# Performance work log

Measured on AMD Instinct MI355X. Metric: run time of the kernel, lower is better.

## Reference

```python
import jax, jax.numpy as jnp
import numpy as np

N_CLUSTERS = 512
TEMPERATURE = 0.1


def setup_inputs() -> dict:
    key = jax.random.key(0)
    k1, k2 = jax.random.split(key)
    x = jax.random.normal(k1, (32, 1024, 256), dtype=jnp.float32)
    centroids = jax.random.normal(k2, (N_CLUSTERS, 256), dtype=jnp.float32)
    return {"x": x, "centroids": centroids}


def reference(x, centroids):
    # Flatten non-cluster axes into a sample axis: [N, D]
    B, S, D = x.shape
    xf = x.reshape(-1, D)  # [N, D]
    x_sq = jnp.sum(xf * xf, axis=-1, keepdims=True)           # [N, 1]
    c_sq = jnp.sum(centroids * centroids, axis=-1)             # [K]
    cross = jnp.einsum('nd,kd->nk', xf, centroids)             # [N, K]
    dists = x_sq - 2.0 * cross + c_sq[None, :]                 # [N, K]
    # Temperature-scaled soft assignments
    assignments = jax.nn.softmax(-dists / TEMPERATURE, axis=-1)  # [N, K]
    # Restore leading (non-feature) dims, append cluster axis
    return assignments.reshape(B, S, N_CLUSTERS)
```

## Files before the change

kernel.cpp:

```cpp
#include <hip/hip_runtime.h>

#define NROWS 32768
#define KC 512
#define DDIM 256
#define BM 128
#define BK 32
#define KCH (DDIM / BK)

typedef __attribute__((ext_vector_type(8))) short bf16x8;
typedef __attribute__((ext_vector_type(4))) float f32x4;

union U8 { unsigned short u[8]; bf16x8 v; };

__device__ __forceinline__ unsigned short f2bf(float f) {
    union { float f; unsigned int u; } a; a.f = f;
    unsigned int r = a.u + 0x7fffu + ((a.u >> 16) & 1u);
    return (unsigned short)(r >> 16);
}
__device__ __forceinline__ float bf2f(unsigned short h) {
    union { unsigned int u; float f; } a; a.u = ((unsigned int)h) << 16;
    return a.f;
}

__global__ __launch_bounds__(64) void prep_c(const float* __restrict__ c,
                                             unsigned short* __restrict__ bhi,
                                             unsigned short* __restrict__ blo,
                                             float* __restrict__ csq10) {
    const int n = blockIdx.x, lane = threadIdx.x;
    const int d0 = lane * 4;
    float4 v = ((const float4*)(c + (size_t)n * DDIM))[lane];
    float vv[4] = {v.x, v.y, v.z, v.w};
    unsigned short hh[4], ll[4];
    float ssq = 0.f;
    #pragma unroll
    for (int i = 0; i < 4; ++i) {
        ssq += vv[i] * vv[i];
        hh[i] = f2bf(vv[i]);
        ll[i] = f2bf(vv[i] - bf2f(hh[i]));
    }
    #pragma unroll
    for (int off = 32; off; off >>= 1) ssq += __shfl_xor(ssq, off);
    if (lane == 0) csq10[n] = 10.f * ssq;
    const int ks = d0 >> 5;
    const int q  = (d0 >> 3) & 3;
    const int t  = n >> 4, cc = n & 15;
    const size_t dst = ((size_t)(ks * 32 + t) * 64 + (q * 16 + cc)) * 8 + (d0 & 7);
    *(ushort4*)(bhi + dst) = make_ushort4(hh[0], hh[1], hh[2], hh[3]);
    *(ushort4*)(blo + dst) = make_ushort4(ll[0], ll[1], ll[2], ll[3]);
}

__global__ __launch_bounds__(512, 2) void kmeans_mfma(
    const float* __restrict__ x, const unsigned short* __restrict__ bhi,
    const unsigned short* __restrict__ blo, const float* __restrict__ csq10,
    float* __restrict__ out) {
    __shared__ __align__(16) float lbuf[32 * 516];
    __shared__ float red[2][2][BM];

    const int tid  = threadIdx.x;
    const int w    = tid >> 6, lane = tid & 63;
    const int wm   = w >> 1, wn = w & 1;
    const int cc   = lane & 15, q = lane >> 4;
    const int row0 = blockIdx.x * BM;

    f32x4 acc[2][16];
    #pragma unroll
    for (int mt = 0; mt < 2; ++mt)
        #pragma unroll
        for (int t = 0; t < 16; ++t) acc[mt][t] = (f32x4){0.f, 0.f, 0.f, 0.f};

    const float* xA0 = x + (size_t)(row0 + wm * 32 + cc) * DDIM + q * 8;
    const float* xA1 = xA0 + (size_t)16 * DDIM;

    float4 c00 = *(const float4*)xA0;
    float4 c01 = *(const float4*)(xA0 + 4);
    float4 c10 = *(const float4*)xA1;
    float4 c11 = *(const float4*)(xA1 + 4);

    for (int ks = 0; ks < KCH; ++ks) {
        float4 n00, n01, n10, n11;
        if (ks < KCH - 1) {
            const int kn = (ks + 1) * BK;
            n00 = *(const float4*)(xA0 + kn);
            n01 = *(const float4*)(xA0 + kn + 4);
            n10 = *(const float4*)(xA1 + kn);
            n11 = *(const float4*)(xA1 + kn + 4);
        }
        bf16x8 ah[2], al[2];
        {
            float v0[8] = {c00.x, c00.y, c00.z, c00.w, c01.x, c01.y, c01.z, c01.w};
            float v1[8] = {c10.x, c10.y, c10.z, c10.w, c11.x, c11.y, c11.z, c11.w};
            U8 H0, L0, H1, L1;
            #pragma unroll
            for (int e = 0; e < 8; ++e) {
                H0.u[e] = f2bf(v0[e]); L0.u[e] = f2bf(v0[e] - bf2f(H0.u[e]));
                H1.u[e] = f2bf(v1[e]); L1.u[e] = f2bf(v1[e] - bf2f(H1.u[e]));
            }
            ah[0] = H0.v; al[0] = L0.v; ah[1] = H1.v; al[1] = L1.v;
        }
        const unsigned short* bhp = bhi + ((size_t)(ks * 32 + wn * 16) << 9) + lane * 8;
        const unsigned short* blp = blo + ((size_t)(ks * 32 + wn * 16) << 9) + lane * 8;
        bf16x8 pb[2][2][2];
        pb[0][0][0] = *(const bf16x8*)(bhp);
        pb[0][0][1] = *(const bf16x8*)(blp);
        pb[0][1][0] = *(const bf16x8*)(bhp + 512);
        pb[0][1][1] = *(const bf16x8*)(blp + 512);
        #pragma unroll
        for (int tg = 0; tg < 8; ++tg) {
            const int par = tg & 1, nxt = par ^ 1;
            if (tg < 7) {
                pb[nxt][0][0] = *(const bf16x8*)(bhp + (2 * tg + 2) * 512);
                pb[nxt][0][1] = *(const bf16x8*)(blp + (2 * tg + 2) * 512);
                pb[nxt][1][0] = *(const bf16x8*)(bhp + (2 * tg + 3) * 512);
                pb[nxt][1][1] = *(const bf16x8*)(blp + (2 * tg + 3) * 512);
            }
            #pragma unroll
            for (int tt = 0; tt < 2; ++tt) {
                const int t = 2 * tg + tt;
                bf16x8 bh = pb[par][tt][0];
                bf16x8 bl = pb[par][tt][1];
                acc[0][t] = __builtin_amdgcn_mfma_f32_16x16x32_bf16(ah[0], bh, acc[0][t], 0, 0, 0);
                acc[1][t] = __builtin_amdgcn_mfma_f32_16x16x32_bf16(ah[1], bh, acc[1][t], 0, 0, 0);
                acc[0][t] = __builtin_amdgcn_mfma_f32_16x16x32_bf16(ah[0], bl, acc[0][t], 0, 0, 0);
                acc[1][t] = __builtin_amdgcn_mfma_f32_16x16x32_bf16(ah[1], bl, acc[1][t], 0, 0, 0);
                acc[0][t] = __builtin_amdgcn_mfma_f32_16x16x32_bf16(al[0], bh, acc[0][t], 0, 0, 0);
                acc[1][t] = __builtin_amdgcn_mfma_f32_16x16x32_bf16(al[1], bh, acc[1][t], 0, 0, 0);
            }
        }
        c00 = n00; c01 = n01; c10 = n10; c11 = n11;
    }

    float csqv[16];
    #pragma unroll
    for (int t = 0; t < 16; ++t) csqv[t] = csq10[wn * 256 + t * 16 + cc];
    const int rb = wm * 32 + q * 4;
    float M[2][4], I[2][4];
    #pragma unroll
    for (int mt = 0; mt < 2; ++mt)
        #pragma unroll
        for (int g = 0; g < 4; ++g) {
            float pm = -1e30f;
            #pragma unroll
            for (int t = 0; t < 16; ++t) pm = fmaxf(pm, 20.f * acc[mt][t][g] - csqv[t]);
            #pragma unroll
            for (int off = 1; off < 16; off <<= 1) pm = fmaxf(pm, __shfl_xor(pm, off));
            if (cc == 0) red[0][wn][rb + mt * 16 + g] = pm;
            M[mt][g] = pm;
        }
    __syncthreads();
    #pragma unroll
    for (int mt = 0; mt < 2; ++mt)
        #pragma unroll
        for (int g = 0; g < 4; ++g) {
            M[mt][g] = fmaxf(M[mt][g], red[0][1 - wn][rb + mt * 16 + g]);
            float ps = 0.f;
            #pragma unroll
            for (int t = 0; t < 16; ++t) ps += __expf(20.f * acc[mt][t][g] - csqv[t] - M[mt][g]);
            #pragma unroll
            for (int off = 1; off < 16; off <<= 1) ps += __shfl_xor(ps, off);
            if (cc == 0) red[1][wn][rb + mt * 16 + g] = ps;
        }
    __syncthreads();
    #pragma unroll
    for (int mt = 0; mt < 2; ++mt)
        #pragma unroll
        for (int g = 0; g < 4; ++g)
            I[mt][g] = 1.f / (red[1][0][rb + mt * 16 + g] + red[1][1][rb + mt * 16 + g]);

    #pragma unroll
    for (int p = 0; p < 4; ++p) {
        if (wm == p) {
            #pragma unroll
            for (int mt = 0; mt < 2; ++mt)
                #pragma unroll
                for (int g = 0; g < 4; ++g) {
                    const int   lr = mt * 16 + q * 4 + g;
                    const float mg = M[mt][g], ig = I[mt][g];
                    #pragma unroll
                    for (int t = 0; t < 16; ++t)
                        lbuf[lr * 516 + wn * 256 + t * 16 + cc] =
                            __expf(20.f * acc[mt][t][g] - csqv[t] - mg) * ig;
                }
        }
        __syncthreads();
        #pragma unroll
        for (int j = 0; j < 8; ++j) {
            const int f    = j * 512 + tid;
            const int lrow = f >> 7;
            const int c4   = f & 127;
            float4    v    = *(const float4*)&lbuf[lrow * 516 + c4 * 4];
            *(float4*)(out + (size_t)(row0 + p * 32 + lrow) * KC + c4 * 4) = v;
        }
        __syncthreads();
    }
}

extern "C" void kernel_launch(void* const* d_in, const int* in_sizes, int n_in,
                              void* d_out, int out_size, void* d_ws, size_t ws_size,
                              hipStream_t stream) {
    const float* x   = (const float*)d_in[0];
    const float* c   = (const float*)d_in[1];
    float*       out = (float*)d_out;

    unsigned short* bhi   = (unsigned short*)d_ws;
    unsigned short* blo   = bhi + (size_t)KCH * KC * BK;
    float*          csq10 = (float*)(blo + (size_t)KCH * KC * BK);

    prep_c<<<KC, 64, 0, stream>>>(c, bhi, blo, csq10);
    kmeans_mfma<<<NROWS / BM, 512, 0, stream>>>(x, bhi, blo, csq10, out);
}
```

Measured before the change: 123.3 us.

## Shrink row tile to 32 with four column-split waves and cross-ks B prefetch

The row block drops from 128 to 32 rows per workgroup, and the workgroup goes from 512 to 256 threads. Each of the four waves now covers 128 centroid columns instead of 256, so 1024 blocks are launched instead of 256, the LDS staging buffer shrinks, and accumulator registers fall by half. The B-fragment double buffer is carried across ks iterations so the next chunk's loads overlap the current MFMAs, and the MFMA issue order is regrouped by precision pass. In exchange, each block reloads the full centroid operand from L2 for only 32 rows, which raises global read traffic, and the softmax reductions now span four waves.

```diff
diff --git a/kernel.cpp b/kernel.cpp
--- a/kernel.cpp
+++ b/kernel.cpp
@@ -3,7 +3,7 @@
 #define NROWS 32768
 #define KC 512
 #define DDIM 256
-#define BM 128
+#define BM 32
 #define BK 32
 #define KCH (DDIM / BK)
 
@@ -49,28 +49,34 @@
     *(ushort4*)(blo + dst) = make_ushort4(ll[0], ll[1], ll[2], ll[3]);
 }
 
-__global__ __launch_bounds__(512, 2) void kmeans_mfma(
+__global__ __launch_bounds__(256, 3) void kmeans_mfma(
     const float* __restrict__ x, const unsigned short* __restrict__ bhi,
     const unsigned short* __restrict__ blo, const float* __restrict__ csq10,
     float* __restrict__ out) {
-    __shared__ __align__(16) float lbuf[32 * 516];
-    __shared__ float red[2][2][BM];
+    __shared__ __align__(16) float lbuf[16 * 516];
+    __shared__ float red[2][4][BM];
 
     const int tid  = threadIdx.x;
-    const int w    = tid >> 6, lane = tid & 63;
-    const int wm   = w >> 1, wn = w & 1;
+    const int wn   = tid >> 6, lane = tid & 63;
     const int cc   = lane & 15, q = lane >> 4;
     const int row0 = blockIdx.x * BM;
 
-    f32x4 acc[2][16];
-    #pragma unroll
-    for (int mt = 0; mt < 2; ++mt)
-        #pragma unroll
-        for (int t = 0; t < 16; ++t) acc[mt][t] = (f32x4){0.f, 0.f, 0.f, 0.f};
-
-    const float* xA0 = x + (size_t)(row0 + wm * 32 + cc) * DDIM + q * 8;
+    f32x4 acc[2][8];
+    #pragma unroll
+    for (int mt = 0; mt < 2; ++mt)
+        #pragma unroll
+        for (int t = 0; t < 8; ++t) acc[mt][t] = (f32x4){0.f, 0.f, 0.f, 0.f};
+
+    const float* xA0 = x + (size_t)(row0 + cc) * DDIM + q * 8;
     const float* xA1 = xA0 + (size_t)16 * DDIM;
 
+    const unsigned short* bhp = bhi + ((size_t)(wn * 8) << 9) + lane * 8;
+    const unsigned short* blp = blo + ((size_t)(wn * 8) << 9) + lane * 8;
+    bf16x8 pb[2][2][2];
+    pb[0][0][0] = *(const bf16x8*)(bhp);
+    pb[0][0][1] = *(const bf16x8*)(blp);
+    pb[0][1][0] = *(const bf16x8*)(bhp + 512);
+    pb[0][1][1] = *(const bf16x8*)(blp + 512);
     float4 c00 = *(const float4*)xA0;
     float4 c01 = *(const float4*)(xA0 + 4);
     float4 c10 = *(const float4*)xA1;
@@ -97,42 +103,41 @@
             }
             ah[0] = H0.v; al[0] = L0.v; ah[1] = H1.v; al[1] = L1.v;
         }
-        const unsigned short* bhp = bhi + ((size_t)(ks * 32 + wn * 16) << 9) + lane * 8;
-        const unsigned short* blp = blo + ((size_t)(ks * 32 + wn * 16) << 9) + lane * 8;
-        bf16x8 pb[2][2][2];
-        pb[0][0][0] = *(const bf16x8*)(bhp);
-        pb[0][0][1] = *(const bf16x8*)(blp);
-        pb[0][1][0] = *(const bf16x8*)(bhp + 512);
-        pb[0][1][1] = *(const bf16x8*)(blp + 512);
-        #pragma unroll
-        for (int tg = 0; tg < 8; ++tg) {
+        #pragma unroll
+        for (int tg = 0; tg < 4; ++tg) {
             const int par = tg & 1, nxt = par ^ 1;
-            if (tg < 7) {
+            if (tg < 3) {
                 pb[nxt][0][0] = *(const bf16x8*)(bhp + (2 * tg + 2) * 512);
                 pb[nxt][0][1] = *(const bf16x8*)(blp + (2 * tg + 2) * 512);
                 pb[nxt][1][0] = *(const bf16x8*)(bhp + (2 * tg + 3) * 512);
                 pb[nxt][1][1] = *(const bf16x8*)(blp + (2 * tg + 3) * 512);
+            } else if (ks < KCH - 1) {
+                pb[nxt][0][0] = *(const bf16x8*)(bhp + 32 * 512);
+                pb[nxt][0][1] = *(const bf16x8*)(blp + 32 * 512);
+                pb[nxt][1][0] = *(const bf16x8*)(bhp + 33 * 512);
+                pb[nxt][1][1] = *(const bf16x8*)(blp + 33 * 512);
             }
             #pragma unroll
-            for (int tt = 0; tt < 2; ++tt) {
-                const int t = 2 * tg + tt;
-                bf16x8 bh = pb[par][tt][0];
-                bf16x8 bl = pb[par][tt][1];
-                acc[0][t] = __builtin_amdgcn_mfma_f32_16x16x32_bf16(ah[0], bh, acc[0][t], 0, 0, 0);
-                acc[1][t] = __builtin_amdgcn_mfma_f32_16x16x32_bf16(ah[1], bh, acc[1][t], 0, 0, 0);
-                acc[0][t] = __builtin_amdgcn_mfma_f32_16x16x32_bf16(ah[0], bl, acc[0][t], 0, 0, 0);
-                acc[1][t] = __builtin_amdgcn_mfma_f32_16x16x32_bf16(ah[1], bl, acc[1][t], 0, 0, 0);
-                acc[0][t] = __builtin_amdgcn_mfma_f32_16x16x32_bf16(al[0], bh, acc[0][t], 0, 0, 0);
-                acc[1][t] = __builtin_amdgcn_mfma_f32_16x16x32_bf16(al[1], bh, acc[1][t], 0, 0, 0);
-            }
-        }
+            for (int p = 0; p < 3; ++p)
+                #pragma unroll
+                for (int tt = 0; tt < 2; ++tt) {
+                    const int t = 2 * tg + tt;
+                    const bf16x8 a0 = (p == 2) ? al[0] : ah[0];
+                    const bf16x8 a1 = (p == 2) ? al[1] : ah[1];
+                    const bf16x8 b  = (p == 1) ? pb[par][tt][1] : pb[par][tt][0];
+                    acc[0][t] = __builtin_amdgcn_mfma_f32_16x16x32_bf16(a0, b, acc[0][t], 0, 0, 0);
+                    acc[1][t] = __builtin_amdgcn_mfma_f32_16x16x32_bf16(a1, b, acc[1][t], 0, 0, 0);
+                }
+        }
+        bhp += 32 * 512;
+        blp += 32 * 512;
         c00 = n00; c01 = n01; c10 = n10; c11 = n11;
     }
 
-    float csqv[16];
-    #pragma unroll
-    for (int t = 0; t < 16; ++t) csqv[t] = csq10[wn * 256 + t * 16 + cc];
-    const int rb = wm * 32 + q * 4;
+    float csqv[8];
+    #pragma unroll
+    for (int t = 0; t < 8; ++t) csqv[t] = csq10[wn * 128 + t * 16 + cc];
+    const int rb = q * 4;
     float M[2][4], I[2][4];
     #pragma unroll
     for (int mt = 0; mt < 2; ++mt)
@@ -140,55 +145,57 @@
         for (int g = 0; g < 4; ++g) {
             float pm = -1e30f;
             #pragma unroll
-            for (int t = 0; t < 16; ++t) pm = fmaxf(pm, 20.f * acc[mt][t][g] - csqv[t]);
+            for (int t = 0; t < 8; ++t) pm = fmaxf(pm, 20.f * acc[mt][t][g] - csqv[t]);
             #pragma unroll
             for (int off = 1; off < 16; off <<= 1) pm = fmaxf(pm, __shfl_xor(pm, off));
             if (cc == 0) red[0][wn][rb + mt * 16 + g] = pm;
-            M[mt][g] = pm;
         }
     __syncthreads();
     #pragma unroll
     for (int mt = 0; mt < 2; ++mt)
         #pragma unroll
         for (int g = 0; g < 4; ++g) {
-            M[mt][g] = fmaxf(M[mt][g], red[0][1 - wn][rb + mt * 16 + g]);
+            const int ri = rb + mt * 16 + g;
+            const float m = fmaxf(fmaxf(red[0][0][ri], red[0][1][ri]),
+                                  fmaxf(red[0][2][ri], red[0][3][ri]));
+            M[mt][g] = m;
             float ps = 0.f;
             #pragma unroll
-            for (int t = 0; t < 16; ++t) ps += __expf(20.f * acc[mt][t][g] - csqv[t] - M[mt][g]);
+            for (int t = 0; t < 8; ++t) ps += __expf(20.f * acc[mt][t][g] - csqv[t] - m);
             #pragma unroll
             for (int off = 1; off < 16; off <<= 1) ps += __shfl_xor(ps, off);
-            if (cc == 0) red[1][wn][rb + mt * 16 + g] = ps;
+            if (cc == 0) red[1][wn][ri] = ps;
         }
     __syncthreads();
     #pragma unroll
     for (int mt = 0; mt < 2; ++mt)
         #pragma unroll
-        for (int g = 0; g < 4; ++g)
-            I[mt][g] = 1.f / (red[1][0][rb + mt * 16 + g] + red[1][1][rb + mt * 16 + g]);
-
-    #pragma unroll
-    for (int p = 0; p < 4; ++p) {
-        if (wm == p) {
-            #pragma unroll
-            for (int mt = 0; mt < 2; ++mt)
-                #pragma unroll
-                for (int g = 0; g < 4; ++g) {
-                    const int   lr = mt * 16 + q * 4 + g;
-                    const float mg = M[mt][g], ig = I[mt][g];
-                    #pragma unroll
-                    for (int t = 0; t < 16; ++t)
-                        lbuf[lr * 516 + wn * 256 + t * 16 + cc] =
-                            __expf(20.f * acc[mt][t][g] - csqv[t] - mg) * ig;
-                }
+        for (int g = 0; g < 4; ++g) {
+            const int ri = rb + mt * 16 + g;
+            I[mt][g] = 1.f / (red[1][0][ri] + red[1][1][ri] +
+                              red[1][2][ri] + red[1][3][ri]);
+        }
+
+    #pragma unroll
+    for (int p = 0; p < 2; ++p) {
+        const int mt = p;
+        #pragma unroll
+        for (int g = 0; g < 4; ++g) {
+            const int   lr = q * 4 + g;
+            const float mg = M[mt][g], ig = I[mt][g];
+            #pragma unroll
+            for (int t = 0; t < 8; ++t)
+                lbuf[lr * 516 + wn * 128 + t * 16 + cc] =
+                    __expf(20.f * acc[mt][t][g] - csqv[t] - mg) * ig;
         }
         __syncthreads();
         #pragma unroll
         for (int j = 0; j < 8; ++j) {
-            const int f    = j * 512 + tid;
+            const int f    = j * 256 + tid;
             const int lrow = f >> 7;
             const int c4   = f & 127;
             float4    v    = *(const float4*)&lbuf[lrow * 516 + c4 * 4];
-            *(float4*)(out + (size_t)(row0 + p * 32 + lrow) * KC + c4 * 4) = v;
+            *(float4*)(out + (size_t)(row0 + p * 16 + lrow) * KC + c4 * 4) = v;
         }
         __syncthreads();
     }
@@ -206,5 +213,5 @@
     float*          csq10 = (float*)(blo + (size_t)KCH * KC * BK);
 
     prep_c<<<KC, 64, 0, stream>>>(c, bhi, blo, csq10);
-    kmeans_mfma<<<NROWS / BM, 512, 0, stream>>>(x, bhi, blo, csq10, out);
-}
+    kmeans_mfma<<<NROWS / BM, 256, 0, stream>>>(x, bhi, blo, csq10, out);
+}
```

Result: slower. 143.1 us (+16.0%).
